# Kernel optimization log

Hardware: AMD Instinct MI355X
Metric: run time of the kernel (lower is better)

The kernel has to match this reference:

```python
import jax, jax.numpy as jnp
import numpy as np

_FP8_DTYPE = jnp.float8_e4m3fn
_FP8_MAX = 448.0  # finfo(float8_e4m3fn).max


def setup_inputs() -> dict:
    key = jax.random.key(0)
    k_x, k_w = jax.random.split(key)
    B, S, IN, OUT = 2, 8192, 2048, 2048
    x = jax.random.normal(k_x, (B, S, IN), dtype=jnp.float32)
    # weight stored in fp8_e4m3fn, per-tensor scalar weight_scale
    w_f32 = jax.random.normal(k_w, (OUT, IN), dtype=jnp.float32) * 0.02
    weight = w_f32.astype(_FP8_DTYPE)
    weight_scale = jnp.asarray(1.5, dtype=jnp.float32)
    input_scale = jnp.asarray(0.75, dtype=jnp.bfloat16)  # bf16 buffer as in torch
    return {"x": x, "weight": weight, "weight_scale": weight_scale, "input_scale": input_scale}


def reference(x, weight, weight_scale, input_scale):
    orig_dtype = x.dtype
    # dequantize fp8 weight: w = fp8 * scale (in original dtype)
    w = weight.astype(orig_dtype) * weight_scale.astype(orig_dtype)
    # static fake-quant of activations: scale -> clamp -> fp8 cast -> dequant
    s_f32 = input_scale.astype(jnp.float32)
    x_scaled = x.astype(jnp.float32) / s_f32
    x_fp8 = jnp.clip(x_scaled, -_FP8_MAX, _FP8_MAX).astype(_FP8_DTYPE)
    x_qdq = x_fp8.astype(orig_dtype) * s_f32.astype(orig_dtype)
    # dense linear: [B,S,IN] @ [OUT,IN]^T -> [B,S,OUT]
    return jnp.einsum("bsi,oi->bso", x_qdq, w)
```

## Files before the change

### kernel.cpp

```cpp
#include <hip/hip_runtime.h>
#include <hip/hip_bf16.h>
#include <stdint.h>

#define M_DIM 16384
#define N_DIM 2048
#define K_DIM 2048

#define BM 128
#define BN 128
#define BK 128
#define NTILES (K_DIM / BK)
#define GRID_M (M_DIM / BM)
#define GRID_N (N_DIM / BN)

typedef float    f32x4 __attribute__((ext_vector_type(4)));
typedef uint32_t u32x4 __attribute__((ext_vector_type(4)));
typedef int      i32x8 __attribute__((ext_vector_type(8)));

#define SCALE_ONE 0x7F7F7F7F

__device__ inline uint32_t quant4(float4 v, float rs) {
    float q0 = fminf(fmaxf(v.x * rs, -448.f), 448.f);
    float q1 = fminf(fmaxf(v.y * rs, -448.f), 448.f);
    float q2 = fminf(fmaxf(v.z * rs, -448.f), 448.f);
    float q3 = fminf(fmaxf(v.w * rs, -448.f), 448.f);
    int p = __builtin_amdgcn_cvt_pk_fp8_f32(q0, q1, 0, false);
    p     = __builtin_amdgcn_cvt_pk_fp8_f32(q2, q3, p, true);
    return (uint32_t)p;
}

__global__ __launch_bounds__(256) void quant_x_kernel(
    const float* __restrict__ x, const float* __restrict__ s_ptr,
    uint32_t* __restrict__ xq)
{
    const float rs = 1.0f / s_ptr[0];
    const float4* xf4 = (const float4*)x;
    const int base = blockIdx.x * 4096 + threadIdx.x;
#pragma unroll
    for (int k = 0; k < 16; ++k) {
        const int i = base + k * 256;
        xq[i] = quant4(xf4[i], rs);
    }
}

__global__ __launch_bounds__(256) void conv_w_kernel(
    const float* __restrict__ w, uint32_t* __restrict__ wq)
{
    const float4* wf4 = (const float4*)w;
    const int base = blockIdx.x * 1024 + threadIdx.x;
#pragma unroll
    for (int k = 0; k < 4; ++k) {
        const int i = base + k * 256;
        wq[i] = quant4(wf4[i], 1.0f);
    }
}

__global__ __launch_bounds__(256) void gemm_mxfp8_kernel(
    const uint8_t* __restrict__ Aq,
    const uint8_t* __restrict__ Wq,
    const float* __restrict__ wscale,
    const float* __restrict__ iscale,
    float* __restrict__ out)
{
    __shared__ uint8_t smA[2][BM * BK];
    __shared__ uint8_t smB[2][BN * BK];

    const int tid  = threadIdx.x;
    const int lane = tid & 63;
    const int wid  = tid >> 6;

    const int bid = blockIdx.x;
    const int wg  = (bid & 7) * (GRID_M * GRID_N / 8) + (bid >> 3);
    const int bm  = wg >> 4;
    const int bn  = wg & 15;
    const int rowBase = bm * BM;
    const int colBase = bn * BN;

    const int wrow = (wid >> 1) * 64;
    const int wcol = (wid & 1) * 64;

    const int srow = lane >> 3;
    const int spos = ((lane & 7) ^ srow) * 16;
    auto stage = [&](int buf, int kt) {
        const int k0 = kt * BK;
#pragma unroll
        for (int j = 0; j < 4; ++j) {
            const int chunk = j * 4 + wid;
            const int row   = chunk * 8 + srow;
            const uint8_t* gA = Aq + (size_t)(rowBase + row) * K_DIM + k0 + spos;
            __builtin_amdgcn_global_load_lds(
                (const __attribute__((address_space(1))) void*)gA,
                (__attribute__((address_space(3))) void*)&smA[buf][chunk * 1024],
                16, 0, 0);
            const uint8_t* gB = Wq + (size_t)(colBase + row) * K_DIM + k0 + spos;
            __builtin_amdgcn_global_load_lds(
                (const __attribute__((address_space(1))) void*)gB,
                (__attribute__((address_space(3))) void*)&smB[buf][chunk * 1024],
                16, 0, 0);
        }
    };

    const int afr   = lane & 15;
    const int rx    = lane & 7;
    const int kblk2 = (lane >> 4) * 2;
    const int p0    = kblk2 ^ rx;

    f32x4 acc[4][4] = {};

    stage(0, 0);
    __syncthreads();

    for (int kt = 0; kt < NTILES; ++kt) {
        const int cur = kt & 1;
        if (kt + 1 < NTILES) stage(cur ^ 1, kt + 1);

        const uint8_t* pA = smA[cur];
        const uint8_t* pB = smB[cur];
        i32x8 av[4], bv[4];
#pragma unroll
        for (int m = 0; m < 4; ++m) {
            const int ro = (wrow + m * 16 + afr) * BK;
            u32x4 lo = *(const u32x4*)(pA + ro + p0 * 16);
            u32x4 hi = *(const u32x4*)(pA + ro + (p0 ^ 1) * 16);
            av[m] = (i32x8){(int)lo.x, (int)lo.y, (int)lo.z, (int)lo.w,
                            (int)hi.x, (int)hi.y, (int)hi.z, (int)hi.w};
        }
#pragma unroll
        for (int n = 0; n < 4; ++n) {
            const int ro = (wcol + n * 16 + afr) * BK;
            u32x4 lo = *(const u32x4*)(pB + ro + p0 * 16);
            u32x4 hi = *(const u32x4*)(pB + ro + (p0 ^ 1) * 16);
            bv[n] = (i32x8){(int)lo.x, (int)lo.y, (int)lo.z, (int)lo.w,
                            (int)hi.x, (int)hi.y, (int)hi.z, (int)hi.w};
        }
#pragma unroll
        for (int m = 0; m < 4; ++m)
#pragma unroll
            for (int n = 0; n < 4; ++n)
                acc[m][n] = __builtin_amdgcn_mfma_scale_f32_16x16x128_f8f6f4(
                    av[m], bv[n], acc[m][n],
                    0 , 0 ,
                    0, SCALE_ONE, 0, SCALE_ONE);
        __syncthreads();
    }

    const float sc = wscale[0] * iscale[0];
    const int crow = (lane >> 4) << 2;
    const int ccol = lane & 15;
#pragma unroll
    for (int m = 0; m < 4; ++m) {
#pragma unroll
        for (int n = 0; n < 4; ++n) {
            const size_t base = (size_t)(rowBase + wrow + m * 16 + crow) * N_DIM
                              + (colBase + wcol + n * 16 + ccol);
#pragma unroll
            for (int r = 0; r < 4; ++r)
                out[base + (size_t)r * N_DIM] = acc[m][n][r] * sc;
        }
    }
}

__global__ __launch_bounds__(256) void fused_fp8_gemm(
    const float* __restrict__ X, const float* __restrict__ Wf,
    const float* __restrict__ wscale, const float* __restrict__ iscale,
    float* __restrict__ out)
{
    __shared__ uint8_t smA[2][128 * 64];
    __shared__ uint8_t smB[2][128 * 64];

    const int tid  = threadIdx.x;
    const int lane = tid & 63;
    const int wid  = tid >> 6;

    const float s  = iscale[0];
    const float rs = 1.0f / s;
    const float sc = wscale[0] * s;

    const int bid = blockIdx.x;
    const int wg  = (bid & 7) * (GRID_M * GRID_N / 8) + (bid >> 3);
    const int bm  = wg >> 4;
    const int bn  = wg & 15;
    const int rowBase = bm * BM;
    const int colBase = bn * BN;
    const int wrow = (wid >> 1) * 64;
    const int wcol = (wid & 1) * 64;
    const int ar = tid >> 1;
    const int ah = (tid & 1) * 32;

    const float* Xrow = X  + (size_t)(rowBase + ar) * K_DIM;
    const float* Wrow = Wf + (size_t)(colBase + ar) * K_DIM;

    float4 areg[8], breg[8];
    auto load_tile = [&](int kt) {
        const int k0 = kt * 64;
#pragma unroll
        for (int j = 0; j < 8; ++j) areg[j] = *(const float4*)(Xrow + k0 + ah + j * 4);
#pragma unroll
        for (int j = 0; j < 8; ++j) breg[j] = *(const float4*)(Wrow + k0 + ah + j * 4);
    };
    auto write_tile = [&](int buf) {
        uint32_t aq[8], bq[8];
#pragma unroll
        for (int j = 0; j < 8; ++j) { aq[j] = quant4(areg[j], rs); bq[j] = quant4(breg[j], 1.0f); }
        *(u32x4*)&smA[buf][ar * 64 + ah]      = *(const u32x4*)&aq[0];
        *(u32x4*)&smA[buf][ar * 64 + ah + 16] = *(const u32x4*)&aq[4];
        *(u32x4*)&smB[buf][ar * 64 + ah]      = *(const u32x4*)&bq[0];
        *(u32x4*)&smB[buf][ar * 64 + ah + 16] = *(const u32x4*)&bq[4];
    };

    f32x4 acc[4][4] = {};
    load_tile(0); write_tile(0); __syncthreads();
    for (int kt = 0; kt < 32; ++kt) {
        const int cur = kt & 1;
        if (kt + 1 < 32) load_tile(kt + 1);
        const uint8_t* pA = smA[cur];
        const uint8_t* pB = smB[cur];
        const int afr = lane & 15, koff = (lane >> 4) << 3;
#pragma unroll
        for (int kk = 0; kk < 2; ++kk) {
            long long a[4], b[4];
#pragma unroll
            for (int m = 0; m < 4; ++m)
                a[m] = *(const long long*)(pA + (wrow + m * 16 + afr) * 64 + kk * 32 + koff);
#pragma unroll
            for (int n = 0; n < 4; ++n)
                b[n] = *(const long long*)(pB + (wcol + n * 16 + afr) * 64 + kk * 32 + koff);
#pragma unroll
            for (int m = 0; m < 4; ++m)
#pragma unroll
                for (int n = 0; n < 4; ++n)
                    acc[m][n] = __builtin_amdgcn_mfma_f32_16x16x32_fp8_fp8(
                        a[m], b[n], acc[m][n], 0, 0, 0);
        }
        if (kt + 1 < 32) write_tile(cur ^ 1);
        __syncthreads();
    }
    const int crow = (lane >> 4) << 2, ccol = lane & 15;
#pragma unroll
    for (int m = 0; m < 4; ++m)
#pragma unroll
        for (int n = 0; n < 4; ++n) {
            const size_t base = (size_t)(rowBase + wrow + m * 16 + crow) * N_DIM
                              + (colBase + wcol + n * 16 + ccol);
#pragma unroll
            for (int r = 0; r < 4; ++r)
                out[base + (size_t)r * N_DIM] = acc[m][n][r] * sc;
        }
}

extern "C" void kernel_launch(void* const* d_in, const int* in_sizes, int n_in,
                              void* d_out, int out_size, void* d_ws, size_t ws_size,
                              hipStream_t stream) {
    const float* x      = (const float*)d_in[0];
    const float* w      = (const float*)d_in[1];
    const float* wscale = (const float*)d_in[2];
    const float* iscale = (const float*)d_in[3];
    float*       out    = (float*)d_out;

    const size_t needA = (size_t)M_DIM * K_DIM;
    const size_t needW = (size_t)N_DIM * K_DIM;
    if (ws_size >= needA + needW) {
        uint32_t* xq = (uint32_t*)d_ws;
        uint32_t* wq = (uint32_t*)((uint8_t*)d_ws + needA);
        quant_x_kernel<<<2048, 256, 0, stream>>>(x, iscale, xq);
        conv_w_kernel<<<1024, 256, 0, stream>>>(w, wq);
        gemm_mxfp8_kernel<<<GRID_M * GRID_N, 256, 0, stream>>>(
            (const uint8_t*)xq, (const uint8_t*)wq, wscale, iscale, out);
    } else {
        fused_fp8_gemm<<<GRID_M * GRID_N, 256, 0, stream>>>(x, w, wscale, iscale, out);
    }
}
```

Measured before the change: 119.3 us.

## Merge quant kernels and use 256x128 triple-buffered 8-wave MX-FP8 GEMM

Merges the activation and weight quantization kernels into a single launch. Replaces the 128x128 double-buffered GEMM with a 256x128 tile per 512-thread block. The new GEMM uses a three-slot dynamic-LDS pipeline with explicit vmcnt/lgkmcnt waits, barriers and s_setprio around the MFMA block. The LDS layout is pre-arranged so each lane reads its MFMA fragment with contiguous 16-byte loads instead of XOR-swizzled addressing. The aims are to hide global-load latency, raise arithmetic intensity per block and drop one launch, at the cost of 144KB LDS with occupancy 1 and a hipFuncSetAttribute call on every launch.

```diff
diff --git a/kernel.cpp b/kernel.cpp
--- a/kernel.cpp
+++ b/kernel.cpp
@@ -5,13 +5,6 @@
 #define M_DIM 16384
 #define N_DIM 2048
 #define K_DIM 2048
-
-#define BM 128
-#define BN 128
-#define BK 128
-#define NTILES (K_DIM / BK)
-#define GRID_M (M_DIM / BM)
-#define GRID_N (N_DIM / BN)
 
 typedef float    f32x4 __attribute__((ext_vector_type(4)));
 typedef uint32_t u32x4 __attribute__((ext_vector_type(4)));
@@ -29,122 +22,149 @@
     return (uint32_t)p;
 }
 
-__global__ __launch_bounds__(256) void quant_x_kernel(
-    const float* __restrict__ x, const float* __restrict__ s_ptr,
-    uint32_t* __restrict__ xq)
+__global__ __launch_bounds__(256) void quant_xw_kernel(
+    const float* __restrict__ x, const float* __restrict__ w,
+    const float* __restrict__ s_ptr,
+    uint32_t* __restrict__ xq, uint32_t* __restrict__ wq)
 {
-    const float rs = 1.0f / s_ptr[0];
-    const float4* xf4 = (const float4*)x;
-    const int base = blockIdx.x * 4096 + threadIdx.x;
-#pragma unroll
-    for (int k = 0; k < 16; ++k) {
-        const int i = base + k * 256;
-        xq[i] = quant4(xf4[i], rs);
-    }
-}
-
-__global__ __launch_bounds__(256) void conv_w_kernel(
-    const float* __restrict__ w, uint32_t* __restrict__ wq)
-{
-    const float4* wf4 = (const float4*)w;
-    const int base = blockIdx.x * 1024 + threadIdx.x;
-#pragma unroll
-    for (int k = 0; k < 4; ++k) {
-        const int i = base + k * 256;
-        wq[i] = quant4(wf4[i], 1.0f);
-    }
-}
-
-__global__ __launch_bounds__(256) void gemm_mxfp8_kernel(
+    if (blockIdx.x < 2048) {
+        const float rs = 1.0f / s_ptr[0];
+        const float4* xf4 = (const float4*)x;
+        const int base = blockIdx.x * 4096 + threadIdx.x;
+#pragma unroll
+        for (int k = 0; k < 16; ++k) {
+            const int i = base + k * 256;
+            xq[i] = quant4(xf4[i], rs);
+        }
+    } else {
+        const float4* wf4 = (const float4*)w;
+        const int base = (blockIdx.x - 2048) * 1024 + threadIdx.x;
+#pragma unroll
+        for (int k = 0; k < 4; ++k) {
+            const int i = base + k * 256;
+            wq[i] = quant4(wf4[i], 1.0f);
+        }
+    }
+}
+
+#define G_BM 256
+#define G_BN 128
+#define G_NT 16
+#define G_GM (M_DIM / G_BM)
+#define G_GN (N_DIM / G_BN)
+#define SLOT 49152
+
+extern __shared__ uint8_t smem[];
+
+__global__ __launch_bounds__(512, 1) void gemm_mx_256(
     const uint8_t* __restrict__ Aq,
     const uint8_t* __restrict__ Wq,
     const float* __restrict__ wscale,
     const float* __restrict__ iscale,
     float* __restrict__ out)
 {
-    __shared__ uint8_t smA[2][BM * BK];
-    __shared__ uint8_t smB[2][BN * BK];
-
     const int tid  = threadIdx.x;
     const int lane = tid & 63;
     const int wid  = tid >> 6;
 
     const int bid = blockIdx.x;
-    const int wg  = (bid & 7) * (GRID_M * GRID_N / 8) + (bid >> 3);
+    const int wg  = (bid & 7) * (G_GM * G_GN / 8) + (bid >> 3);
     const int bm  = wg >> 4;
     const int bn  = wg & 15;
-    const int rowBase = bm * BM;
-    const int colBase = bn * BN;
+    const int rowBase = bm * G_BM;
+    const int colBase = bn * G_BN;
+
+    const float scv = wscale[0] * iscale[0];
+    asm volatile("" :: "v"(scv));
+
+    const uint8_t* gsrc[6];
+    int ldsoff[6];
+#pragma unroll
+    for (int j = 0; j < 6; ++j) {
+        const int iss = wid + j * 8;
+        const int jj  = iss & 1;
+        const int col = (lane >> 4) * 32 + jj * 16;
+        int row; const uint8_t* base; int lo;
+        if (iss < 32) {
+            row  = rowBase + (iss >> 3) * 64 + ((iss >> 1) & 3) * 16 + (lane & 15);
+            base = Aq;  lo = iss * 1024;
+        } else {
+            const int pb = iss - 32;
+            row  = colBase + (pb >> 3) * 64 + ((pb >> 1) & 3) * 16 + (lane & 15);
+            base = Wq;  lo = 32768 + pb * 1024;
+        }
+        gsrc[j]   = base + (size_t)row * K_DIM + col;
+        ldsoff[j] = lo;
+    }
+
+    auto stage = [&](int slot, int tt) {
+        const size_t koff = (size_t)tt * 128;
+        uint8_t* sb = smem + slot * SLOT;
+#pragma unroll
+        for (int j = 0; j < 6; ++j)
+            __builtin_amdgcn_global_load_lds(
+                (const __attribute__((address_space(1))) void*)(gsrc[j] + koff),
+                (__attribute__((address_space(3))) void*)(sb + ldsoff[j]),
+                16, 0, 0);
+    };
+
+    const int aBase = (wid >> 1) * 8192;
+    const int bBase = 32768 + (wid & 1) * 8192;
+    const int l16   = lane * 16;
+
+    f32x4 acc[4][4] = {};
+
+    stage(0, 0); stage(1, 1); stage(2, 2);
+    asm volatile("s_waitcnt vmcnt(12)" ::: "memory");
+    __builtin_amdgcn_s_barrier();
+    __builtin_amdgcn_sched_barrier(0);
+
+    for (int t = 0; t < G_NT; ++t) {
+        const int slot = t % 3;
+        const uint8_t* sb = smem + slot * SLOT;
+
+        u32x4 aLo[4], aHi[4], bLo[4], bHi[4];
+#pragma unroll
+        for (int m = 0; m < 4; ++m) {
+            aLo[m] = *(const u32x4*)(sb + aBase + m * 2048 + l16);
+            aHi[m] = *(const u32x4*)(sb + aBase + m * 2048 + 1024 + l16);
+        }
+#pragma unroll
+        for (int n = 0; n < 4; ++n) {
+            bLo[n] = *(const u32x4*)(sb + bBase + n * 2048 + l16);
+            bHi[n] = *(const u32x4*)(sb + bBase + n * 2048 + 1024 + l16);
+        }
+        __builtin_amdgcn_sched_barrier(0);
+        asm volatile("s_waitcnt lgkmcnt(0)" ::: "memory");
+        __builtin_amdgcn_s_barrier();
+        __builtin_amdgcn_sched_barrier(0);
+
+        stage(slot, (t + 3 > G_NT - 1) ? G_NT - 1 : t + 3);
+        __builtin_amdgcn_sched_barrier(0);
+
+        __builtin_amdgcn_s_setprio(1);
+#pragma unroll
+        for (int m = 0; m < 4; ++m) {
+            const i32x8 av = {(int)aLo[m].x, (int)aLo[m].y, (int)aLo[m].z, (int)aLo[m].w,
+                              (int)aHi[m].x, (int)aHi[m].y, (int)aHi[m].z, (int)aHi[m].w};
+#pragma unroll
+            for (int n = 0; n < 4; ++n) {
+                const i32x8 bv = {(int)bLo[n].x, (int)bLo[n].y, (int)bLo[n].z, (int)bLo[n].w,
+                                  (int)bHi[n].x, (int)bHi[n].y, (int)bHi[n].z, (int)bHi[n].w};
+                acc[m][n] = __builtin_amdgcn_mfma_scale_f32_16x16x128_f8f6f4(
+                    av, bv, acc[m][n], 0, 0, 0, SCALE_ONE, 0, SCALE_ONE);
+            }
+        }
+        __builtin_amdgcn_s_setprio(0);
+        __builtin_amdgcn_sched_barrier(0);
+
+        asm volatile("s_waitcnt vmcnt(12)" ::: "memory");
+        __builtin_amdgcn_s_barrier();
+        __builtin_amdgcn_sched_barrier(0);
+    }
 
     const int wrow = (wid >> 1) * 64;
     const int wcol = (wid & 1) * 64;
-
-    const int srow = lane >> 3;
-    const int spos = ((lane & 7) ^ srow) * 16;
-    auto stage = [&](int buf, int kt) {
-        const int k0 = kt * BK;
-#pragma unroll
-        for (int j = 0; j < 4; ++j) {
-            const int chunk = j * 4 + wid;
-            const int row   = chunk * 8 + srow;
-            const uint8_t* gA = Aq + (size_t)(rowBase + row) * K_DIM + k0 + spos;
-            __builtin_amdgcn_global_load_lds(
-                (const __attribute__((address_space(1))) void*)gA,
-                (__attribute__((address_space(3))) void*)&smA[buf][chunk * 1024],
-                16, 0, 0);
-            const uint8_t* gB = Wq + (size_t)(colBase + row) * K_DIM + k0 + spos;
-            __builtin_amdgcn_global_load_lds(
-                (const __attribute__((address_space(1))) void*)gB,
-                (__attribute__((address_space(3))) void*)&smB[buf][chunk * 1024],
-                16, 0, 0);
-        }
-    };
-
-    const int afr   = lane & 15;
-    const int rx    = lane & 7;
-    const int kblk2 = (lane >> 4) * 2;
-    const int p0    = kblk2 ^ rx;
-
-    f32x4 acc[4][4] = {};
-
-    stage(0, 0);
-    __syncthreads();
-
-    for (int kt = 0; kt < NTILES; ++kt) {
-        const int cur = kt & 1;
-        if (kt + 1 < NTILES) stage(cur ^ 1, kt + 1);
-
-        const uint8_t* pA = smA[cur];
-        const uint8_t* pB = smB[cur];
-        i32x8 av[4], bv[4];
-#pragma unroll
-        for (int m = 0; m < 4; ++m) {
-            const int ro = (wrow + m * 16 + afr) * BK;
-            u32x4 lo = *(const u32x4*)(pA + ro + p0 * 16);
-            u32x4 hi = *(const u32x4*)(pA + ro + (p0 ^ 1) * 16);
-            av[m] = (i32x8){(int)lo.x, (int)lo.y, (int)lo.z, (int)lo.w,
-                            (int)hi.x, (int)hi.y, (int)hi.z, (int)hi.w};
-        }
-#pragma unroll
-        for (int n = 0; n < 4; ++n) {
-            const int ro = (wcol + n * 16 + afr) * BK;
-            u32x4 lo = *(const u32x4*)(pB + ro + p0 * 16);
-            u32x4 hi = *(const u32x4*)(pB + ro + (p0 ^ 1) * 16);
-            bv[n] = (i32x8){(int)lo.x, (int)lo.y, (int)lo.z, (int)lo.w,
-                            (int)hi.x, (int)hi.y, (int)hi.z, (int)hi.w};
-        }
-#pragma unroll
-        for (int m = 0; m < 4; ++m)
-#pragma unroll
-            for (int n = 0; n < 4; ++n)
-                acc[m][n] = __builtin_amdgcn_mfma_scale_f32_16x16x128_f8f6f4(
-                    av[m], bv[n], acc[m][n],
-                    0 , 0 ,
-                    0, SCALE_ONE, 0, SCALE_ONE);
-        __syncthreads();
-    }
-
-    const float sc = wscale[0] * iscale[0];
     const int crow = (lane >> 4) << 2;
     const int ccol = lane & 15;
 #pragma unroll
@@ -155,7 +175,7 @@
                               + (colBase + wcol + n * 16 + ccol);
 #pragma unroll
             for (int r = 0; r < 4; ++r)
-                out[base + (size_t)r * N_DIM] = acc[m][n][r] * sc;
+                out[base + (size_t)r * N_DIM] = acc[m][n][r] * scv;
         }
     }
 }
@@ -177,11 +197,11 @@
     const float sc = wscale[0] * s;
 
     const int bid = blockIdx.x;
-    const int wg  = (bid & 7) * (GRID_M * GRID_N / 8) + (bid >> 3);
+    const int wg  = (bid & 7) * 256 + (bid >> 3);
     const int bm  = wg >> 4;
     const int bn  = wg & 15;
-    const int rowBase = bm * BM;
-    const int colBase = bn * BN;
+    const int rowBase = bm * 128;
+    const int colBase = bn * 128;
     const int wrow = (wid >> 1) * 64;
     const int wcol = (wid & 1) * 64;
     const int ar = tid >> 1;
@@ -259,14 +279,18 @@
 
     const size_t needA = (size_t)M_DIM * K_DIM;
     const size_t needW = (size_t)N_DIM * K_DIM;
-    if (ws_size >= needA + needW) {
+
+    hipError_t e = hipFuncSetAttribute((const void*)gemm_mx_256,
+                                       hipFuncAttributeMaxDynamicSharedMemorySize,
+                                       3 * SLOT);
+
+    if (e == hipSuccess && ws_size >= needA + needW) {
         uint32_t* xq = (uint32_t*)d_ws;
         uint32_t* wq = (uint32_t*)((uint8_t*)d_ws + needA);
-        quant_x_kernel<<<2048, 256, 0, stream>>>(x, iscale, xq);
-        conv_w_kernel<<<1024, 256, 0, stream>>>(w, wq);
-        gemm_mxfp8_kernel<<<GRID_M * GRID_N, 256, 0, stream>>>(
+        quant_xw_kernel<<<3072, 256, 0, stream>>>(x, w, iscale, xq, wq);
+        gemm_mx_256<<<G_GM * G_GN, 512, 3 * SLOT, stream>>>(
             (const uint8_t*)xq, (const uint8_t*)wq, wscale, iscale, out);
     } else {
-        fused_fp8_gemm<<<GRID_M * GRID_N, 256, 0, stream>>>(x, w, wscale, iscale, out);
-    }
-}
+        fused_fp8_gemm<<<2048, 256, 0, stream>>>(x, w, wscale, iscale, out);
+    }
+}
```

Result: slower. 159.1 us (+33.3%).
